# Kernel tuning notes

Hardware: AMD Instinct MI355X
Metric: run time of the kernel (lower is better)

The kernel has to match this reference:

```python
import jax, jax.numpy as jnp
import numpy as np

N_NODES = 100000
D = 128


def _sage_layer(h, src, dst, w_self, w_neigh, b):
    # GraphSAGE mean aggregation: mean of neighbor (src) features per dst node.
    msg = h[src]                                            # [E, D] gather
    agg = jax.ops.segment_sum(msg, dst, num_segments=N_NODES)  # [N, D]
    deg = jax.ops.segment_sum(jnp.ones(src.shape, h.dtype), dst, num_segments=N_NODES)
    mean = agg / jnp.maximum(deg, 1.0)[:, None]
    return h @ w_self + mean @ w_neigh + b


def setup_inputs() -> dict:
    key = jax.random.key(0)
    ks = jax.random.split(key, 16)
    E = 1600000
    inp = {
        "feat": jax.random.normal(ks[0], (N_NODES, D), jnp.float32),
        "edge0_src": jax.random.randint(ks[1], (E,), 0, N_NODES),
        "edge0_dst": jax.random.randint(ks[2], (E,), 0, N_NODES),
        "edge1_src": jax.random.randint(ks[3], (E,), 0, N_NODES),
        "edge1_dst": jax.random.randint(ks[4], (E,), 0, N_NODES),
        "pos_src": jax.random.randint(ks[5], (100000,), 0, N_NODES),
        "pos_dst": jax.random.randint(ks[6], (100000,), 0, N_NODES),
        "neg_src": jax.random.randint(ks[7], (500000,), 0, N_NODES),
        "neg_dst": jax.random.randint(ks[8], (500000,), 0, N_NODES),
        # learned parameters
        "w_proj": jax.random.normal(ks[9], (D, D), jnp.float32) / np.sqrt(D),
        "b_proj": jnp.zeros((D,), jnp.float32),
        "w_self1": jax.random.normal(ks[10], (D, D), jnp.float32) / np.sqrt(D),
        "w_neigh1": jax.random.normal(ks[11], (D, D), jnp.float32) / np.sqrt(D),
        "b1": jnp.zeros((D,), jnp.float32),
        "w_self2": jax.random.normal(ks[12], (D, D), jnp.float32) / np.sqrt(D),
        "w_neigh2": jax.random.normal(ks[13], (D, D), jnp.float32) / np.sqrt(D),
        "b2": jnp.zeros((D,), jnp.float32),
    }
    return inp


def reference(feat, edge0_src, edge0_dst, edge1_src, edge1_dst,
              pos_src, pos_dst, neg_src, neg_dst,
              w_proj, b_proj, w_self1, w_neigh1, b1, w_self2, w_neigh2, b2):
    # ProjectionLayer: per-node linear + ReLU on blocks[0].srcdata['feature']
    h = jax.nn.relu(feat @ w_proj + b_proj)
    # GNNLayer: one SAGE-mean layer per block
    h = jax.nn.relu(_sage_layer(h, edge0_src, edge0_dst, w_self1, w_neigh1, b1))
    h = _sage_layer(h, edge1_src, edge1_dst, w_self2, w_neigh2, b2)
    # PredictionLayer: dot-product edge scoring on pos_graph / neg_graph
    pos_score = jnp.sum(h[pos_src] * h[pos_dst], axis=-1)
    neg_score = jnp.sum(h[neg_src] * h[neg_dst], axis=-1)
    return (pos_score, neg_score)
```

## Files before the change

kernel.cpp:

```cpp
#include <hip/hip_runtime.h>
#include <hip/hip_bf16.h>

#define NN 100000
#define DD 128

#define NPB 512
#define NB 196
#define CAPB 12288
#define PA_BLOCKS 196

typedef unsigned short ushort_t;
typedef unsigned int uint_t;
typedef __attribute__((ext_vector_type(8))) short bf16x8;
typedef __attribute__((ext_vector_type(4))) float f32x4;

__device__ __forceinline__ ushort_t f2bf(float f) {
    uint_t u = __builtin_bit_cast(uint_t, f);
    u += 0x7FFFu + ((u >> 16) & 1u);
    return (ushort_t)(u >> 16);
}
__device__ __forceinline__ uint_t pack2bf(float a, float b) {
    return (uint_t)f2bf(a) | ((uint_t)f2bf(b) << 16);
}
__device__ __forceinline__ float bflo(uint_t v) {
    return __builtin_bit_cast(float, v << 16);
}
__device__ __forceinline__ float bfhi(uint_t v) {
    return __builtin_bit_cast(float, v & 0xFFFF0000u);
}

#define PREP_W_BLOCKS 320
#define PREP_Z_BLOCKS 2
__global__ __launch_bounds__(256) void prep(
    const float* __restrict__ w_proj,
    const float* __restrict__ w_self1, const float* __restrict__ w_neigh1,
    const float* __restrict__ w_self2, const float* __restrict__ w_neigh2,
    ushort_t* __restrict__ wtp, ushort_t* __restrict__ wt1,
    ushort_t* __restrict__ wt2, int* __restrict__ bcnt)
{
    const int bid = blockIdx.x;
    const int tid = threadIdx.x;
    if (bid < PREP_W_BLOCKS) {
        int which = bid >> 6;
        int t = (bid & 63) * 256 + tid;
        int n = t >> 7, k = t & 127;
        float v;
        ushort_t* d;
        switch (which) {
            case 0: v = w_proj  [(size_t)k * 128 + n]; d = wtp + (size_t)n * 128 + k;       break;
            case 1: v = w_self1 [(size_t)k * 128 + n]; d = wt1 + (size_t)n * 256 + k;       break;
            case 2: v = w_neigh1[(size_t)k * 128 + n]; d = wt1 + (size_t)n * 256 + 128 + k; break;
            case 3: v = w_self2 [(size_t)k * 128 + n]; d = wt2 + (size_t)n * 256 + k;       break;
            default:v = w_neigh2[(size_t)k * 128 + n]; d = wt2 + (size_t)n * 256 + 128 + k; break;
        }
        *d = f2bf(v);
    } else {
        int i = (bid - PREP_W_BLOCKS) * 256 + tid;
        if (i < 2 * NB) bcnt[i] = 0;
    }
}

template <bool RELU, bool TWO, bool CVT>
__global__ __launch_bounds__(256, 4) void gemm_bf16(
    const void* __restrict__ Av, const ushort_t* __restrict__ Bm,
    const ushort_t* __restrict__ W, const float* __restrict__ bias,
    ushort_t* __restrict__ outp)
{
    __shared__ char smem[32768];
    ushort_t* At = (ushort_t*)smem;
    ushort_t* Wt = (ushort_t*)(smem + 10240);
    ushort_t* Ot = (ushort_t*)smem;

    const int tid  = threadIdx.x;
    const int lane = tid & 63;
    const int wav  = tid >> 6;
    const int row0 = blockIdx.x * 128;
    const int m0   = (wav & 1) * 64;
    const int n0   = (wav >> 1) * 64;
    const int KTOT = TWO ? 256 : 128;
    const int NCH  = TWO ? 8 : 4;

    f32x4 acc[4][4];
#pragma unroll
    for (int i = 0; i < 4; ++i)
#pragma unroll
        for (int j = 0; j < 4; ++j) acc[i][j] = (f32x4){0.f, 0.f, 0.f, 0.f};

    const int cl = lane & 15;
    const int q  = lane >> 4;

#pragma unroll 1
    for (int ch = 0; ch < NCH; ++ch) {
        const bool second = TWO && (ch >= 4);
        const int kA = (ch & 3) * 32;
        const int kW = ch * 32;

        uint4 av[2], wv[2];
#pragma unroll
        for (int j = 0; j < 2; ++j) {
            int g = tid + 256 * j;
            int r = g >> 2;
            int c = (g & 3) * 8;
            int grow = row0 + r;
            if (grow >= NN) grow = NN - 1;
            if constexpr (CVT) {
                const float* fp = (const float*)Av;
                float4 f0 = *(const float4*)(fp + (size_t)grow * DD + kA + c);
                float4 f1 = *(const float4*)(fp + (size_t)grow * DD + kA + c + 4);
                av[j].x = pack2bf(f0.x, f0.y);
                av[j].y = pack2bf(f0.z, f0.w);
                av[j].z = pack2bf(f1.x, f1.y);
                av[j].w = pack2bf(f1.z, f1.w);
            } else {
                const ushort_t* sp = second ? Bm : (const ushort_t*)Av;
                av[j] = *(const uint4*)(sp + (size_t)grow * DD + kA + c);
            }
            wv[j] = *(const uint4*)(W + (size_t)r * KTOT + kW + c);
        }
        if (ch) __syncthreads();
#pragma unroll
        for (int j = 0; j < 2; ++j) {
            int g = tid + 256 * j;
            int r = g >> 2;
            int c = (g & 3) * 8;
            *(uint4*)(&At[r * 40 + c]) = av[j];
            *(uint4*)(&Wt[r * 40 + c]) = wv[j];
        }
        __syncthreads();

        bf16x8 af[4], bfr[4];
#pragma unroll
        for (int i = 0; i < 4; ++i)
            af[i] = *(const bf16x8*)(&At[(m0 + i * 16 + cl) * 40 + q * 8]);
#pragma unroll
        for (int j = 0; j < 4; ++j)
            bfr[j] = *(const bf16x8*)(&Wt[(n0 + j * 16 + cl) * 40 + q * 8]);
#pragma unroll
        for (int i = 0; i < 4; ++i)
#pragma unroll
            for (int j = 0; j < 4; ++j)
                acc[i][j] = __builtin_amdgcn_mfma_f32_16x16x32_bf16(
                    af[i], bfr[j], acc[i][j], 0, 0, 0);
    }

    __syncthreads();
#pragma unroll
    for (int j = 0; j < 4; ++j) {
        int c = n0 + j * 16 + cl;
        float bv = bias[c];
#pragma unroll
        for (int i = 0; i < 4; ++i) {
#pragma unroll
            for (int reg = 0; reg < 4; ++reg) {
                int r = m0 + i * 16 + 4 * q + reg;
                float v = acc[i][j][reg] + bv;
                if constexpr (RELU) v = fmaxf(v, 0.f);
                Ot[r * 128 + c] = f2bf(v);
            }
        }
    }
    __syncthreads();
    int rows = NN - row0; if (rows > 128) rows = 128;
    for (int t = tid; t < rows * 16; t += 256) {
        int r = t >> 4, c8 = (t & 15) * 8;
        *(uint4*)(outp + (size_t)(row0 + r) * DD + c8) =
            *(const uint4*)(&Ot[r * 128 + c8]);
    }
}

__global__ __launch_bounds__(256) void partA2(
    const int* __restrict__ e0s, const int* __restrict__ e0d, int E0,
    const int* __restrict__ e1s, const int* __restrict__ e1d, int E1,
    int* __restrict__ bcnt, uint_t* __restrict__ pairs)
{
    __shared__ int hist[NB];
    __shared__ int base[NB];
    const int tid  = threadIdx.x;
    const int half = blockIdx.x >= PA_BLOCKS;
    const int* __restrict__ src = half ? e1s : e0s;
    const int* __restrict__ dst = half ? e1d : e0d;
    const int E = half ? E1 : E0;
    int* bc = bcnt + half * NB;
    uint_t* pp = pairs + (size_t)half * NB * CAPB;
    const int blk = blockIdx.x - half * PA_BLOCKS;
    const int chunk = (E + PA_BLOCKS - 1) / PA_BLOCKS;
    const int ea = blk * chunk;
    int eb = ea + chunk; if (eb > E) eb = E;

    for (int b = tid; b < NB; b += 256) hist[b] = 0;
    __syncthreads();
    for (int e = ea + tid; e < eb; e += 256)
        atomicAdd(&hist[dst[e] >> 9], 1);
    __syncthreads();
    for (int b = tid; b < NB; b += 256) {
        base[b] = atomicAdd(&bc[b], hist[b]);
        hist[b] = 0;
    }
    __syncthreads();
    for (int e = ea + tid; e < eb; e += 256) {
        int d = dst[e];
        int b = d >> 9;
        int off = atomicAdd(&hist[b], 1);
        int p = base[b] + off;
        if (p < CAPB)
            pp[(size_t)b * CAPB + p] =
                ((uint_t)(d & (NPB - 1)) << 17) | (uint_t)src[e];
    }
}

__global__ __launch_bounds__(256, 2) void partB(
    uint_t* __restrict__ pairs, const int* __restrict__ bcnt,
    int* __restrict__ counts, int* __restrict__ offs)
{
    __shared__ int cnt[NPB];
    __shared__ int loff[NPB];
    __shared__ int ssc[256];
    __shared__ int image[CAPB];

    const int tid  = threadIdx.x;
    const int half = blockIdx.x >= NB;
    const int b    = blockIdx.x - half * NB;
    const int n0   = b << 9;
    int nb = NN - n0; if (nb > NPB) nb = NPB;
    int tot = bcnt[half * NB + b]; if (tot > CAPB) tot = CAPB;
    uint_t* pb = pairs + (size_t)(half * NB + b) * CAPB;
    const int gbase = (half * NB + b) * CAPB;
    int* cnts  = counts + (size_t)half * NN;
    int* offsl = offs   + (size_t)half * NN;

    for (int n = tid; n < NPB; n += 256) cnt[n] = 0;
    __syncthreads();
    for (int i = tid; i < tot; i += 256)
        atomicAdd(&cnt[pb[i] >> 17], 1);
    __syncthreads();

    int a0 = cnt[2 * tid], a1 = cnt[2 * tid + 1];
    int s = a0 + a1;
    ssc[tid] = s;
    __syncthreads();
    for (int off = 1; off < 256; off <<= 1) {
        int t = 0;
        if (tid >= off) t = ssc[tid - off];
        __syncthreads();
        if (tid >= off) ssc[tid] += t;
        __syncthreads();
    }
    int pre = ssc[tid] - s;
    loff[2 * tid]     = pre;
    loff[2 * tid + 1] = pre + a0;
    __syncthreads();

    for (int n = tid; n < nb; n += 256) {
        cnts[n0 + n]  = cnt[n];
        offsl[n0 + n] = gbase + loff[n];
    }
    for (int n = tid; n < NPB; n += 256) cnt[n] = 0;
    __syncthreads();

    for (int i = tid; i < tot; i += 256) {
        uint_t p = pb[i];
        int ln  = p >> 17;
        int pos = loff[ln] + atomicAdd(&cnt[ln], 1);
        image[pos] = (int)(p & 0x1FFFFu);
    }
    __syncthreads();
    for (int i = tid; i < tot; i += 256) pb[i] = (uint_t)image[i];
}

#define AGG_ISSUE(V, J)                                                   \
    do {                                                                  \
        int s_[8];                                                        \
        _Pragma("unroll")                                                 \
        for (int u = 0; u < 8; ++u) {                                     \
            int jj = (J) + u;                                             \
            if (jj >= cnt) jj = cnt - 1;                                  \
            s_[u] = (int)csr[start + jj];                                 \
        }                                                                 \
        _Pragma("unroll")                                                 \
        for (int u = 0; u < 8; ++u)                                       \
            V[u] = *(const uint4*)(hl + (size_t)s_[u] * DD);              \
    } while (0)

#define AGG_ACCUM(V, J)                                                   \
    do {                                                                  \
        _Pragma("unroll")                                                 \
        for (int u = 0; u < 8; ++u) {                                     \
            if ((J) + u < cnt) {                                          \
                a0 += bflo(V[u].x); a1 += bfhi(V[u].x);                   \
                a2 += bflo(V[u].y); a3 += bfhi(V[u].y);                   \
                a4 += bflo(V[u].z); a5 += bfhi(V[u].z);                   \
                a6 += bflo(V[u].w); a7 += bfhi(V[u].w);                   \
            }                                                             \
        }                                                                 \
    } while (0)

__global__ __launch_bounds__(256) void aggregate_bf16(
    const ushort_t* __restrict__ h, const uint_t* __restrict__ csr,
    const int* __restrict__ offs, const int* __restrict__ counts,
    ushort_t* __restrict__ mean, int nn)
{
    int gid  = blockIdx.x * 256 + threadIdx.x;
    int node = gid >> 4;
    if (node >= nn) return;
    int lane  = gid & 15;
    int start = offs[node];
    int cnt   = counts[node];
    const ushort_t* __restrict__ hl = h + lane * 8;

    float a0 = 0.f, a1 = 0.f, a2 = 0.f, a3 = 0.f;
    float a4 = 0.f, a5 = 0.f, a6 = 0.f, a7 = 0.f;

    int nbt = (cnt + 7) >> 3;
    if (nbt > 0) {
        uint4 va[8], vb[8];
        AGG_ISSUE(va, 0);
        int ja = 0, j = 8, b = 1;
        for (; b + 1 < nbt; b += 2) {
            int jb = j;
            AGG_ISSUE(vb, jb); j += 8;
            AGG_ACCUM(va, ja);
            ja = j;
            AGG_ISSUE(va, ja); j += 8;
            AGG_ACCUM(vb, jb);
        }
        if (b < nbt) {
            int jb = j;
            AGG_ISSUE(vb, jb);
            AGG_ACCUM(va, ja);
            AGG_ACCUM(vb, jb);
        } else {
            AGG_ACCUM(va, ja);
        }
    }

    float rinv = 1.0f / (float)(cnt > 1 ? cnt : 1);
    uint4 o;
    o.x = pack2bf(a0 * rinv, a1 * rinv);
    o.y = pack2bf(a2 * rinv, a3 * rinv);
    o.z = pack2bf(a4 * rinv, a5 * rinv);
    o.w = pack2bf(a6 * rinv, a7 * rinv);
    *(uint4*)(mean + (size_t)node * DD + lane * 8) = o;
}

__device__ __forceinline__ float dot8(uint4 a, uint4 b) {
    return bflo(a.x) * bflo(b.x) + bfhi(a.x) * bfhi(b.x)
         + bflo(a.y) * bflo(b.y) + bfhi(a.y) * bfhi(b.y)
         + bflo(a.z) * bflo(b.z) + bfhi(a.z) * bfhi(b.z)
         + bflo(a.w) * bflo(b.w) + bfhi(a.w) * bfhi(b.w);
}

__global__ __launch_bounds__(256) void score_both(
    const ushort_t* __restrict__ h,
    const int* __restrict__ ps, const int* __restrict__ pd,
    const int* __restrict__ ns, const int* __restrict__ nd,
    float* __restrict__ out, int EP, int TE)
{
    int gid = blockIdx.x * 256 + threadIdx.x;
    int grp = gid >> 4;
    int e0 = grp * 2;
    if (e0 >= TE) return;
    int lane = gid & 15;
    int e1 = e0 + 1;
    bool has1 = (e1 < TE);
    int ee = has1 ? e1 : e0;

    int s0, d0, s1, d1;
    if (e0 < EP) { s0 = ps[e0]; d0 = pd[e0]; }
    else         { s0 = ns[e0 - EP]; d0 = nd[e0 - EP]; }
    if (ee < EP) { s1 = ps[ee]; d1 = pd[ee]; }
    else         { s1 = ns[ee - EP]; d1 = nd[ee - EP]; }

    const ushort_t* __restrict__ hl = h + lane * 8;
    uint4 va0 = *(const uint4*)(hl + (size_t)s0 * DD);
    uint4 vb0 = *(const uint4*)(hl + (size_t)d0 * DD);
    uint4 va1 = *(const uint4*)(hl + (size_t)s1 * DD);
    uint4 vb1 = *(const uint4*)(hl + (size_t)d1 * DD);

    float r0 = dot8(va0, vb0);
    float r1 = dot8(va1, vb1);
#pragma unroll
    for (int off = 8; off; off >>= 1) {
        r0 += __shfl_down(r0, off, 16);
        r1 += __shfl_down(r1, off, 16);
    }
    if (lane == 0) {
        out[e0] = r0;
        if (has1) out[e1] = r1;
    }
}


extern "C" void kernel_launch(void* const* d_in, const int* in_sizes, int n_in,
                              void* d_out, int out_size, void* d_ws, size_t ws_size,
                              hipStream_t stream)
{
    const float* feat    = (const float*)d_in[0];
    const int*   e0s     = (const int*)d_in[1];
    const int*   e0d     = (const int*)d_in[2];
    const int*   e1s     = (const int*)d_in[3];
    const int*   e1d     = (const int*)d_in[4];
    const int*   ps      = (const int*)d_in[5];
    const int*   pd      = (const int*)d_in[6];
    const int*   ns      = (const int*)d_in[7];
    const int*   nd      = (const int*)d_in[8];
    const float* w_proj  = (const float*)d_in[9];
    const float* b_proj  = (const float*)d_in[10];
    const float* w_self1 = (const float*)d_in[11];
    const float* w_neigh1= (const float*)d_in[12];
    const float* b1      = (const float*)d_in[13];
    const float* w_self2 = (const float*)d_in[14];
    const float* w_neigh2= (const float*)d_in[15];
    const float* b2      = (const float*)d_in[16];

    float* out = (float*)d_out;

    const size_t NF = (size_t)NN * DD;
    char* base = (char*)d_ws;

    ushort_t* h3   = (ushort_t*)base;
    ushort_t* h1   = (ushort_t*)(base + NF * 2);
    ushort_t* mean = (ushort_t*)(base + NF * 4);
    ushort_t* h2   = (ushort_t*)(base + NF * 6);

    uint_t* pairs  = (uint_t*)(base + NF * 8);
    int*    bcnt   = (int*)(pairs + (size_t)2 * NB * CAPB);
    int*    counts = bcnt + 2 * NB;
    int*    offs   = counts + 2 * NN;
    ushort_t* wts  = (ushort_t*)(offs + 2 * NN);
    ushort_t* wtp = wts;
    ushort_t* wt1 = wts + 128 * 128;
    ushort_t* wt2 = wt1 + 128 * 256;

    const int E0 = in_sizes[1];
    const int E1 = in_sizes[3];
    const int EP = in_sizes[5];
    const int EN = in_sizes[7];

    const int GB  = (NN + 127) / 128;
    const int AGB = (NN * 16 + 255) / 256;

    prep<<<PREP_W_BLOCKS + PREP_Z_BLOCKS, 256, 0, stream>>>(
        w_proj, w_self1, w_neigh1, w_self2, w_neigh2, wtp, wt1, wt2, bcnt);

    partA2<<<2 * PA_BLOCKS, 256, 0, stream>>>(
        e0s, e0d, E0, e1s, e1d, E1, bcnt, pairs);
    partB<<<2 * NB, 256, 0, stream>>>(pairs, bcnt, counts, offs);

    gemm_bf16<true, false, true><<<GB, 256, 0, stream>>>(
        feat, nullptr, wtp, b_proj, h1);

    aggregate_bf16<<<AGB, 256, 0, stream>>>(h1, pairs, offs, counts, mean, NN);
    gemm_bf16<true, true, false><<<GB, 256, 0, stream>>>(
        h1, mean, wt1, b1, h2);

    aggregate_bf16<<<AGB, 256, 0, stream>>>(
        h2, pairs, offs + NN, counts + NN, mean, NN);
    gemm_bf16<false, true, false><<<GB, 256, 0, stream>>>(
        h2, mean, wt2, b2, h3);

    const int TE = EP + EN;
    const int NG = (TE + 1) / 2;
    score_both<<<(NG * 16 + 255) / 256, 256, 0, stream>>>(
        h3, ps, pd, ns, nd, out, EP, TE);
}
```

Before: 462.1 us.

## Use direct global-to-LDS loads in GEMM and zero-pad rows for branchless aggregation

The GEMM tile loads now use global_load_lds to copy A and W chunks straight into LDS, skipping the round trip through registers, and the LDS row stride drops from 40 to 32 to fit the direct-copy layout. Separately, h1 and h2 each get one extra zero row at index NN. Aggregation tail slots now point at that row, so the per-element bounds checks in the accumulate loop go away. The unpadded stride may bring back LDS bank conflicts on the MFMA fragment reads, and the workspace layout shifts to make room for the padding rows.

```diff
diff --git a/kernel.cpp b/kernel.cpp
--- a/kernel.cpp
+++ b/kernel.cpp
@@ -29,14 +29,22 @@
     return __builtin_bit_cast(float, v & 0xFFFF0000u);
 }
 
+__device__ __forceinline__ void gload16(const ushort_t* g, ushort_t* l) {
+    __builtin_amdgcn_global_load_lds(
+        (const __attribute__((address_space(1))) void*)g,
+        (__attribute__((address_space(3))) void*)l,
+        16, 0, 0);
+}
+
 #define PREP_W_BLOCKS 320
-#define PREP_Z_BLOCKS 2
+#define PREP_Z_BLOCKS 3
 __global__ __launch_bounds__(256) void prep(
     const float* __restrict__ w_proj,
     const float* __restrict__ w_self1, const float* __restrict__ w_neigh1,
     const float* __restrict__ w_self2, const float* __restrict__ w_neigh2,
     ushort_t* __restrict__ wtp, ushort_t* __restrict__ wt1,
-    ushort_t* __restrict__ wt2, int* __restrict__ bcnt)
+    ushort_t* __restrict__ wt2, int* __restrict__ bcnt,
+    ushort_t* __restrict__ h1pad, ushort_t* __restrict__ h2pad)
 {
     const int bid = blockIdx.x;
     const int tid = threadIdx.x;
@@ -54,9 +62,14 @@
             default:v = w_neigh2[(size_t)k * 128 + n]; d = wt2 + (size_t)n * 256 + 128 + k; break;
         }
         *d = f2bf(v);
-    } else {
+    } else if (bid < PREP_W_BLOCKS + 2) {
         int i = (bid - PREP_W_BLOCKS) * 256 + tid;
         if (i < 2 * NB) bcnt[i] = 0;
+    } else {
+        uint_t* p1 = (uint_t*)h1pad;
+        uint_t* p2 = (uint_t*)h2pad;
+        if (tid < 64) p1[tid] = 0;
+        else if (tid < 128) p2[tid - 64] = 0;
     }
 }
 
@@ -68,7 +81,7 @@
 {
     __shared__ char smem[32768];
     ushort_t* At = (ushort_t*)smem;
-    ushort_t* Wt = (ushort_t*)(smem + 10240);
+    ushort_t* Wt = (ushort_t*)(smem + 8192);
     ushort_t* Ot = (ushort_t*)smem;
 
     const int tid  = threadIdx.x;
@@ -95,46 +108,61 @@
         const int kA = (ch & 3) * 32;
         const int kW = ch * 32;
 
-        uint4 av[2], wv[2];
-#pragma unroll
-        for (int j = 0; j < 2; ++j) {
-            int g = tid + 256 * j;
-            int r = g >> 2;
-            int c = (g & 3) * 8;
-            int grow = row0 + r;
-            if (grow >= NN) grow = NN - 1;
-            if constexpr (CVT) {
-                const float* fp = (const float*)Av;
+        if (ch) __syncthreads();
+
+        if constexpr (CVT) {
+#pragma unroll
+            for (int j = 0; j < 2; ++j) {
+                int cb = (j * 4 + wav) * 64;
+                int c  = cb + lane;
+                int r  = c >> 2, k2 = c & 3;
+                gload16(W + (size_t)r * KTOT + kW + k2 * 8, Wt + cb * 8);
+            }
+            uint4 av[2];
+            const float* fp = (const float*)Av;
+#pragma unroll
+            for (int j = 0; j < 2; ++j) {
+                int g = tid + 256 * j;
+                int r = g >> 2;
+                int c = (g & 3) * 8;
+                int grow = row0 + r;
+                if (grow >= NN) grow = NN - 1;
                 float4 f0 = *(const float4*)(fp + (size_t)grow * DD + kA + c);
                 float4 f1 = *(const float4*)(fp + (size_t)grow * DD + kA + c + 4);
                 av[j].x = pack2bf(f0.x, f0.y);
                 av[j].y = pack2bf(f0.z, f0.w);
                 av[j].z = pack2bf(f1.x, f1.y);
                 av[j].w = pack2bf(f1.z, f1.w);
-            } else {
-                const ushort_t* sp = second ? Bm : (const ushort_t*)Av;
-                av[j] = *(const uint4*)(sp + (size_t)grow * DD + kA + c);
             }
-            wv[j] = *(const uint4*)(W + (size_t)r * KTOT + kW + c);
-        }
-        if (ch) __syncthreads();
-#pragma unroll
-        for (int j = 0; j < 2; ++j) {
-            int g = tid + 256 * j;
-            int r = g >> 2;
-            int c = (g & 3) * 8;
-            *(uint4*)(&At[r * 40 + c]) = av[j];
-            *(uint4*)(&Wt[r * 40 + c]) = wv[j];
+#pragma unroll
+            for (int j = 0; j < 2; ++j) {
+                int g = tid + 256 * j;
+                int r = g >> 2;
+                int c = (g & 3) * 8;
+                *(uint4*)(&At[r * 32 + c]) = av[j];
+            }
+        } else {
+            const ushort_t* sp = second ? Bm : (const ushort_t*)Av;
+#pragma unroll
+            for (int j = 0; j < 2; ++j) {
+                int cb = (j * 4 + wav) * 64;
+                int c  = cb + lane;
+                int r  = c >> 2, k2 = c & 3;
+                int grow = row0 + r;
+                if (grow >= NN) grow = NN - 1;
+                gload16(sp + (size_t)grow * DD + kA + k2 * 8, At + cb * 8);
+                gload16(W + (size_t)r * KTOT + kW + k2 * 8, Wt + cb * 8);
+            }
         }
         __syncthreads();
 
         bf16x8 af[4], bfr[4];
 #pragma unroll
         for (int i = 0; i < 4; ++i)
-            af[i] = *(const bf16x8*)(&At[(m0 + i * 16 + cl) * 40 + q * 8]);
+            af[i] = *(const bf16x8*)(&At[(m0 + i * 16 + cl) * 32 + q * 8]);
 #pragma unroll
         for (int j = 0; j < 4; ++j)
-            bfr[j] = *(const bf16x8*)(&Wt[(n0 + j * 16 + cl) * 40 + q * 8]);
+            bfr[j] = *(const bf16x8*)(&Wt[(n0 + j * 16 + cl) * 32 + q * 8]);
 #pragma unroll
         for (int i = 0; i < 4; ++i)
 #pragma unroll
@@ -273,24 +301,23 @@
         _Pragma("unroll")                                                 \
         for (int u = 0; u < 8; ++u) {                                     \
             int jj = (J) + u;                                             \
-            if (jj >= cnt) jj = cnt - 1;                                  \
-            s_[u] = (int)csr[start + jj];                                 \
+            int jc = jj < cnt ? jj : cnt - 1;                             \
+            int sv = (int)csr[start + jc];                                \
+            s_[u] = jj < cnt ? sv : NN;                                   \
         }                                                                 \
         _Pragma("unroll")                                                 \
         for (int u = 0; u < 8; ++u)                                       \
             V[u] = *(const uint4*)(hl + (size_t)s_[u] * DD);              \
     } while (0)
 
-#define AGG_ACCUM(V, J)                                                   \
+#define AGG_ACCUM(V)                                                      \
     do {                                                                  \
         _Pragma("unroll")                                                 \
         for (int u = 0; u < 8; ++u) {                                     \
-            if ((J) + u < cnt) {                                          \
-                a0 += bflo(V[u].x); a1 += bfhi(V[u].x);                   \
-                a2 += bflo(V[u].y); a3 += bfhi(V[u].y);                   \
-                a4 += bflo(V[u].z); a5 += bfhi(V[u].z);                   \
-                a6 += bflo(V[u].w); a7 += bfhi(V[u].w);                   \
-            }                                                             \
+            a0 += bflo(V[u].x); a1 += bfhi(V[u].x);                       \
+            a2 += bflo(V[u].y); a3 += bfhi(V[u].y);                       \
+            a4 += bflo(V[u].z); a5 += bfhi(V[u].z);                       \
+            a6 += bflo(V[u].w); a7 += bfhi(V[u].w);                       \
         }                                                                 \
     } while (0)
 
@@ -314,22 +341,19 @@
     if (nbt > 0) {
         uint4 va[8], vb[8];
         AGG_ISSUE(va, 0);
-        int ja = 0, j = 8, b = 1;
+        int j = 8, b = 1;
         for (; b + 1 < nbt; b += 2) {
-            int jb = j;
-            AGG_ISSUE(vb, jb); j += 8;
-            AGG_ACCUM(va, ja);
-            ja = j;
-            AGG_ISSUE(va, ja); j += 8;
-            AGG_ACCUM(vb, jb);
+            AGG_ISSUE(vb, j); j += 8;
+            AGG_ACCUM(va);
+            AGG_ISSUE(va, j); j += 8;
+            AGG_ACCUM(vb);
         }
         if (b < nbt) {
-            int jb = j;
-            AGG_ISSUE(vb, jb);
-            AGG_ACCUM(va, ja);
-            AGG_ACCUM(vb, jb);
+            AGG_ISSUE(vb, j);
+            AGG_ACCUM(va);
+            AGG_ACCUM(vb);
         } else {
-            AGG_ACCUM(va, ja);
+            AGG_ACCUM(va);
         }
     }
 
@@ -414,15 +438,16 @@
 
     float* out = (float*)d_out;
 
-    const size_t NF = (size_t)NN * DD;
+    const size_t NF  = (size_t)NN * DD;
+    const size_t NFP = NF + DD;
     char* base = (char*)d_ws;
 
     ushort_t* h3   = (ushort_t*)base;
-    ushort_t* h1   = (ushort_t*)(base + NF * 2);
-    ushort_t* mean = (ushort_t*)(base + NF * 4);
-    ushort_t* h2   = (ushort_t*)(base + NF * 6);
-
-    uint_t* pairs  = (uint_t*)(base + NF * 8);
+    ushort_t* h1   = h3 + NFP;
+    ushort_t* mean = h1 + NFP;
+    ushort_t* h2   = mean + NFP;
+
+    uint_t* pairs  = (uint_t*)(h2 + NFP);
     int*    bcnt   = (int*)(pairs + (size_t)2 * NB * CAPB);
     int*    counts = bcnt + 2 * NB;
     int*    offs   = counts + 2 * NN;
@@ -440,7 +465,8 @@
     const int AGB = (NN * 16 + 255) / 256;
 
     prep<<<PREP_W_BLOCKS + PREP_Z_BLOCKS, 256, 0, stream>>>(
-        w_proj, w_self1, w_neigh1, w_self2, w_neigh2, wtp, wt1, wt2, bcnt);
+        w_proj, w_self1, w_neigh1, w_self2, w_neigh2, wtp, wt1, wt2, bcnt,
+        h1 + NF, h2 + NF);
 
     partA2<<<2 * PA_BLOCKS, 256, 0, stream>>>(
         e0s, e0d, E0, e1s, e1d, E1, bcnt, pairs);
```

Measured after the change: 402.6 us. -12.9%, faster.
